# Kernel optimization log

Measured on AMD Instinct MI355X. Metric: run time of the kernel, lower is better.

The kernel has to match this reference:

```python
import jax, jax.numpy as jnp
import numpy as np

N_NODES = 100000
N_EDGES = 600000
NUM_GRAPHS = 512
IN_DIM = 128
HID = 64
HEADS = 2
NEG_SLOPE = 0.2


def gat_layer(h_in, src, dst, W, a_s, a_d, b, n_nodes):
    # W: [F_in, H*C], a_s/a_d: [H, C], b: [H*C]
    H, C = a_s.shape
    h = (h_in @ W).reshape(n_nodes, H, C)            # [N,H,C]
    alpha_src = jnp.einsum('nhc,hc->nh', h, a_s)      # [N,H]
    alpha_dst = jnp.einsum('nhc,hc->nh', h, a_d)      # [N,H]
    e = alpha_src[src] + alpha_dst[dst]               # [E,H]
    e = jnp.where(e >= 0, e, NEG_SLOPE * e)           # leaky_relu
    # segment softmax over destination node
    m = jax.ops.segment_max(e, dst, num_segments=n_nodes)
    m = jnp.where(jnp.isfinite(m), m, 0.0)
    ex = jnp.exp(e - m[dst])                          # [E,H]
    denom = jax.ops.segment_sum(ex, dst, num_segments=n_nodes)
    alpha = ex / jnp.maximum(denom[dst], 1e-16)       # [E,H]
    out = jax.ops.segment_sum(alpha[:, :, None] * h[src], dst, num_segments=n_nodes)
    return out.reshape(n_nodes, H * C) + b


def setup_inputs() -> dict:
    key = jax.random.key(0)
    ks = jax.random.split(key, 16)
    x = jax.random.normal(ks[0], (N_NODES, IN_DIM), dtype=jnp.float32)
    edge_index = jax.random.randint(ks[1], (2, N_EDGES), 0, N_NODES, dtype=jnp.int32)
    batch = jnp.sort(jax.random.randint(ks[2], (N_NODES,), 0, NUM_GRAPHS, dtype=jnp.int32))
    s = lambda *d: 1.0 / np.sqrt(d[0])
    W1 = jax.random.normal(ks[3], (IN_DIM, HEADS * HID), jnp.float32) * s(IN_DIM)
    a_src1 = jax.random.normal(ks[4], (HEADS, HID), jnp.float32) * s(HID)
    a_dst1 = jax.random.normal(ks[5], (HEADS, HID), jnp.float32) * s(HID)
    b1 = jnp.zeros((HEADS * HID,), jnp.float32)
    W2 = jax.random.normal(ks[6], (HEADS * HID, HID), jnp.float32) * s(HEADS * HID)
    a_src2 = jax.random.normal(ks[7], (1, HID), jnp.float32) * s(HID)
    a_dst2 = jax.random.normal(ks[8], (1, HID), jnp.float32) * s(HID)
    b2 = jnp.zeros((HID,), jnp.float32)
    Wf1 = jax.random.normal(ks[9], (2 * HID, HID), jnp.float32) * s(2 * HID)
    bf1 = jnp.zeros((HID,), jnp.float32)
    Wf2 = jax.random.normal(ks[10], (HID, 1), jnp.float32) * s(HID)
    bf2 = jnp.zeros((1,), jnp.float32)
    return dict(x=x, edge_index=edge_index, batch=batch, W1=W1, a_src1=a_src1,
                a_dst1=a_dst1, b1=b1, W2=W2, a_src2=a_src2, a_dst2=a_dst2, b2=b2,
                Wf1=Wf1, bf1=bf1, Wf2=Wf2, bf2=bf2)


def reference(x, edge_index, batch, W1, a_src1, a_dst1, b1, W2, a_src2, a_dst2, b2,
              Wf1, bf1, Wf2, bf2):
    n = x.shape[0]
    loops = jnp.arange(n, dtype=edge_index.dtype)
    src = jnp.concatenate([edge_index[0], loops])
    dst = jnp.concatenate([edge_index[1], loops])
    h = gat_layer(x, src, dst, W1, a_src1, a_dst1, b1, n)
    h = jax.nn.relu(h)
    h = gat_layer(h, src, dst, W2, a_src2, a_dst2, b2, n)  # [N, HID]
    # global mean + max pool per graph
    ones = jnp.ones((n,), h.dtype)
    counts = jax.ops.segment_sum(ones, batch, num_segments=NUM_GRAPHS)  # [G]
    mean = jax.ops.segment_sum(h, batch, num_segments=NUM_GRAPHS) / jnp.maximum(counts, 1.0)[:, None]
    mx = jax.ops.segment_max(h, batch, num_segments=NUM_GRAPHS)
    mx = jnp.where(counts[:, None] > 0, mx, 0.0)
    pooled = jnp.concatenate([mean, mx], axis=1)  # [G, 2*HID]
    out = jax.nn.relu(pooled @ Wf1 + bf1) @ Wf2 + bf2  # [G, 1]
    return out
```

## Files before the change

### kernel.cpp

```cpp
#include <hip/hip_runtime.h>

#define N_NODESC 100000
#define N_EDGESC 600000
#define E_TOTC   700000
#define NUM_GRAPHSC 512
#define NEG_SLOPE 0.2f
#define NEG_INF_ENC 0x007FFFFFu
#define SCAN_NB 128

typedef unsigned short ushort_t;
typedef __attribute__((ext_vector_type(8))) short bf16x8;
typedef __attribute__((ext_vector_type(4))) float f32x4;

__device__ __forceinline__ unsigned enc_f32(float f) {
    unsigned u = __float_as_uint(f);
    return (u & 0x80000000u) ? ~u : (u | 0x80000000u);
}
__device__ __forceinline__ float dec_f32(unsigned u) {
    u = (u & 0x80000000u) ? (u ^ 0x80000000u) : ~u;
    return __uint_as_float(u);
}
__device__ __forceinline__ ushort_t f32_to_bf16(float f) {
    unsigned u = __float_as_uint(f);
    return (ushort_t)((u + 0x7FFFu + ((u >> 16) & 1u)) >> 16);
}
__device__ __forceinline__ float bf16_to_f32(ushort_t h) {
    return __uint_as_float(((unsigned)h) << 16);
}
__device__ __forceinline__ unsigned pack_bf16x2(float a, float b) {
    return (unsigned)f32_to_bf16(a) | ((unsigned)f32_to_bf16(b) << 16);
}

__global__ __launch_bounds__(256) void init_all(float* __restrict__ msum,
                                                unsigned* __restrict__ mmax,
                                                float* __restrict__ cnt,
                                                int* __restrict__ deg,
                                                const float* __restrict__ W1,
                                                const float* __restrict__ W2,
                                                ushort_t* __restrict__ wPre1,
                                                ushort_t* __restrict__ wPre2) {
    int i = blockIdx.x * 256 + threadIdx.x;
    if (i < NUM_GRAPHSC * 64) { msum[i] = 0.f; mmax[i] = NEG_INF_ENC; }
    if (i < NUM_GRAPHSC) cnt[i] = 0.f;
    if (i < N_NODESC) deg[i] = 0;
    if (i < 128 * 128) {
        int n = i >> 7, k = i & 127;
        wPre1[n * 128 + k] = f32_to_bf16(W1[k * 128 + n]);
    } else if (i < 128 * 128 + 64 * 128) {
        int j = i - 128 * 128;
        int n = j >> 7, k = j & 127;
        wPre2[n * 128 + k] = f32_to_bf16(W2[k * 64 + n]);
    }
}

__global__ __launch_bounds__(256) void hist_dst(const int* __restrict__ ei,
                                                int* __restrict__ deg) {
    int e = blockIdx.x * blockDim.x + threadIdx.x;
    if (e >= E_TOTC) return;
    int d = (e < N_EDGESC) ? ei[N_EDGESC + e] : e - N_EDGESC;
    atomicAdd(&deg[d], 1);
}

__global__ __launch_bounds__(256) void scan_partial(const int* __restrict__ deg,
                                                    int* __restrict__ bsum, int n) {
    __shared__ int red[256];
    int chunk = (n + SCAN_NB - 1) / SCAN_NB;
    int lo = blockIdx.x * chunk, hi = min(lo + chunk, n);
    int s = 0;
    for (int i = lo + threadIdx.x; i < hi; i += 256) s += deg[i];
    red[threadIdx.x] = s;
    __syncthreads();
    for (int d = 128; d; d >>= 1) {
        if (threadIdx.x < d) red[threadIdx.x] += red[threadIdx.x + d];
        __syncthreads();
    }
    if (threadIdx.x == 0) bsum[blockIdx.x] = red[0];
}

__global__ __launch_bounds__(256) void scan_final(const int* __restrict__ deg,
                                                  const int* __restrict__ bsum,
                                                  int* __restrict__ off, int n) {
    __shared__ int bs[SCAN_NB];
    __shared__ int tile[256];
    __shared__ int carry;
    int t = threadIdx.x;
    if (t < SCAN_NB) bs[t] = bsum[t];
    __syncthreads();
    for (int d = 1; d < SCAN_NB; d <<= 1) {
        int v = (t >= d && t < SCAN_NB) ? bs[t - d] : 0;
        __syncthreads();
        if (t < SCAN_NB) bs[t] += v;
        __syncthreads();
    }
    if (t == 0) carry = blockIdx.x ? bs[blockIdx.x - 1] : 0;
    __syncthreads();
    int chunk = (n + SCAN_NB - 1) / SCAN_NB;
    int lo = blockIdx.x * chunk, hi = min(lo + chunk, n);
    for (int base = lo; base < hi; base += 256) {
        int i = base + t;
        int v = (i < hi) ? deg[i] : 0;
        tile[t] = v;
        __syncthreads();
        for (int d = 1; d < 256; d <<= 1) {
            int u = (t >= d) ? tile[t - d] : 0;
            __syncthreads();
            tile[t] += u;
            __syncthreads();
        }
        if (i < hi) off[i] = carry + tile[t] - v;
        __syncthreads();
        if (t == 0) carry += tile[255];
        __syncthreads();
    }
}

__global__ __launch_bounds__(256) void scatter_csr(const int* __restrict__ ei,
                                                   int* __restrict__ off,
                                                   int* __restrict__ csr) {
    int e = blockIdx.x * blockDim.x + threadIdx.x;
    if (e >= E_TOTC) return;
    int s, d;
    if (e < N_EDGESC) { s = ei[e]; d = ei[N_EDGESC + e]; } else { s = d = e - N_EDGESC; }
    int slot = atomicAdd(&off[d], 1);
    csr[slot] = s;
}

__global__ __launch_bounds__(256) void gemm1_mfma(const float* __restrict__ X,
                                                  const ushort_t* __restrict__ Wp,
                                                  ushort_t* __restrict__ Y16, int N) {
    int tid = threadIdx.x;
    int wave = tid >> 6, lane = tid & 63;
    int quad = lane >> 4, l16 = lane & 15;
    size_t node0 = (size_t)blockIdx.x * 64;

    f32x4 acc[4][2];
#pragma unroll
    for (int rt = 0; rt < 4; ++rt)
#pragma unroll
        for (int ct = 0; ct < 2; ++ct) acc[rt][ct] = (f32x4){0.f, 0.f, 0.f, 0.f};

    const ushort_t* w0p = Wp + (size_t)(16 * wave + l16) * 128;
    const ushort_t* w1p = Wp + (size_t)(64 + 16 * wave + l16) * 128;

#pragma unroll
    for (int kc = 0; kc < 4; ++kc) {
        int kb = kc * 32 + quad * 8;
        float4 xa[4], xb[4];
#pragma unroll
        for (int rt = 0; rt < 4; ++rt) {
            size_t row = node0 + rt * 16 + l16;
            if (row >= (size_t)N) row = N - 1;
            const float* xp = X + row * 128 + kb;
            xa[rt] = *(const float4*)xp;
            xb[rt] = *(const float4*)(xp + 4);
        }
        bf16x8 b0 = *(const bf16x8*)(w0p + kb);
        bf16x8 b1 = *(const bf16x8*)(w1p + kb);
#pragma unroll
        for (int rt = 0; rt < 4; ++rt) {
            union { bf16x8 v; unsigned u[4]; } af;
            af.u[0] = pack_bf16x2(xa[rt].x, xa[rt].y);
            af.u[1] = pack_bf16x2(xa[rt].z, xa[rt].w);
            af.u[2] = pack_bf16x2(xb[rt].x, xb[rt].y);
            af.u[3] = pack_bf16x2(xb[rt].z, xb[rt].w);
            acc[rt][0] = __builtin_amdgcn_mfma_f32_16x16x32_bf16(af.v, b0, acc[rt][0], 0, 0, 0);
            acc[rt][1] = __builtin_amdgcn_mfma_f32_16x16x32_bf16(af.v, b1, acc[rt][1], 0, 0, 0);
        }
    }
    unsigned* Yu = (unsigned*)Y16;
    int c = 16 * wave + l16;
#pragma unroll
    for (int rt = 0; rt < 4; ++rt)
#pragma unroll
        for (int r = 0; r < 4; ++r) {
            size_t row = node0 + rt * 16 + quad * 4 + r;
            if (row < (size_t)N)
                Yu[row * 64 + c] = pack_bf16x2(acc[rt][0][r], acc[rt][1][r]);
        }
}

__global__ __launch_bounds__(256) void gemm2_mfma(const ushort_t* __restrict__ Xb,
                                                  const ushort_t* __restrict__ Wp,
                                                  ushort_t* __restrict__ Y16, int N) {
    int tid = threadIdx.x;
    int wave = tid >> 6, lane = tid & 63;
    int quad = lane >> 4, l16 = lane & 15;
    int rbase = (wave >> 1) * 32, cbase = (wave & 1) * 32;
    size_t node0 = (size_t)blockIdx.x * 64;

    bf16x8 a[2][4];
#pragma unroll
    for (int rt = 0; rt < 2; ++rt) {
        size_t row = node0 + rbase + rt * 16 + l16;
        if (row >= (size_t)N) row = N - 1;
#pragma unroll
        for (int kc = 0; kc < 4; ++kc)
            a[rt][kc] = *(const bf16x8*)(Xb + row * 128 + kc * 32 + quad * 8);
    }

    const ushort_t* b0p = Wp + (size_t)(cbase + l16) * 128;
    const ushort_t* b1p = Wp + (size_t)(cbase + 16 + l16) * 128;

    f32x4 acc[2][2];
#pragma unroll
    for (int rt = 0; rt < 2; ++rt)
#pragma unroll
        for (int ct = 0; ct < 2; ++ct) acc[rt][ct] = (f32x4){0.f, 0.f, 0.f, 0.f};

#pragma unroll
    for (int kc = 0; kc < 4; ++kc) {
        int kb = kc * 32 + quad * 8;
        bf16x8 b0 = *(const bf16x8*)(b0p + kb);
        bf16x8 b1 = *(const bf16x8*)(b1p + kb);
#pragma unroll
        for (int rt = 0; rt < 2; ++rt) {
            acc[rt][0] = __builtin_amdgcn_mfma_f32_16x16x32_bf16(a[rt][kc], b0, acc[rt][0], 0, 0, 0);
            acc[rt][1] = __builtin_amdgcn_mfma_f32_16x16x32_bf16(a[rt][kc], b1, acc[rt][1], 0, 0, 0);
        }
    }
#pragma unroll
    for (int rt = 0; rt < 2; ++rt)
#pragma unroll
        for (int ct = 0; ct < 2; ++ct)
#pragma unroll
            for (int r = 0; r < 4; ++r) {
                size_t row = node0 + rbase + rt * 16 + quad * 4 + r;
                if (row < (size_t)N)
                    Y16[row * 64 + cbase + ct * 16 + l16] = f32_to_bf16(acc[rt][ct][r]);
            }
}

template <int H>
__global__ __launch_bounds__(256) void node_alpha(const ushort_t* __restrict__ H16,
                                                  const float* __restrict__ a_s,
                                                  const float* __restrict__ a_d,
                                                  float* __restrict__ as_out,
                                                  float* __restrict__ ad_out, int N) {
    int wid = threadIdx.x >> 6, lane = threadIdx.x & 63;
    int n = blockIdx.x * 4 + wid;
    if (n >= N) return;
    if (H == 2) {
        const unsigned* hrow = (const unsigned*)(H16 + (size_t)n * 128);
        unsigned u = hrow[lane];
        float h0 = __uint_as_float(u << 16);
        float h1 = __uint_as_float(u & 0xffff0000u);
        float ps0 = h0 * a_s[lane], pd0 = h0 * a_d[lane];
        float ps1 = h1 * a_s[64 + lane], pd1 = h1 * a_d[64 + lane];
#pragma unroll
        for (int off = 32; off; off >>= 1) {
            ps0 += __shfl_xor(ps0, off);
            pd0 += __shfl_xor(pd0, off);
            ps1 += __shfl_xor(ps1, off);
            pd1 += __shfl_xor(pd1, off);
        }
        if (lane == 0) {
            as_out[n * 2 + 0] = ps0; ad_out[n * 2 + 0] = pd0;
            as_out[n * 2 + 1] = ps1; ad_out[n * 2 + 1] = pd1;
        }
    } else {
        float hv = bf16_to_f32(H16[(size_t)n * 64 + lane]);
        float ps = hv * a_s[lane];
        float pd = hv * a_d[lane];
#pragma unroll
        for (int off = 32; off; off >>= 1) {
            ps += __shfl_xor(ps, off);
            pd += __shfl_xor(pd, off);
        }
        if (lane == 0) { as_out[n] = ps; ad_out[n] = pd; }
    }
}

template <int H, bool RELU, bool OB16>
__global__ __launch_bounds__(256) void gat_gather(const int* __restrict__ off_end,
                                                  const int* __restrict__ deg,
                                                  const int* __restrict__ csr,
                                                  const float* __restrict__ as,
                                                  const float* __restrict__ ad,
                                                  const ushort_t* __restrict__ H16,
                                                  const float* __restrict__ b,
                                                  void* __restrict__ outp, int N) {
    int lane = threadIdx.x & 63;
    int wave = threadIdx.x >> 6;
    int l = lane & 15;
    int gbase = lane & 48;
    int n = blockIdx.x * 16 + wave * 4 + (lane >> 4);
    if (n >= N) return;
    int dg = deg[n];
    int o = off_end[n] - dg;
    float adv[H];
#pragma unroll
    for (int h = 0; h < H; ++h) adv[h] = ad[n * H + h];

    float acc[H][4], den[H];
#pragma unroll
    for (int h = 0; h < H; ++h) {
        den[h] = 0.f;
#pragma unroll
        for (int q = 0; q < 4; ++q) acc[h][q] = 0.f;
    }

    const unsigned* Hu = (const unsigned*)H16;

    for (int base = 0; base < dg; base += 16) {
        int i = base + l;
        bool valid = i < dg;
        int s = valid ? csr[o + i] : 0;
        float v[H];
        if (H == 2) {
            float2 p = valid ? ((const float2*)as)[s] : make_float2(0.f, 0.f);
            v[0] = p.x + adv[0];
            v[H - 1] = p.y + adv[H - 1];
        } else {
            v[0] = valid ? as[s] + adv[0] : 0.f;
        }
#pragma unroll
        for (int h = 0; h < H; ++h) {
            float e = v[h] >= 0.f ? v[h] : NEG_SLOPE * v[h];
            v[h] = valid ? __expf(e) : 0.f;
            den[h] += v[h];
        }
        int wpk = (H == 2) ? (int)pack_bf16x2(v[0], v[H - 1])
                           : (int)__float_as_uint(v[0]);
        int cnt = min(dg - base, 16);
        int cnt4 = (cnt + 3) & ~3;
        for (int j = 0; j < cnt4; j += 4) {
#pragma unroll
            for (int u = 0; u < 4; ++u) {
                int src = gbase + j + u;
                int sj = __shfl(s, src);
                int wp = __shfl(wpk, src);
                if (H == 2) {
                    float w0 = __uint_as_float(((unsigned)wp) << 16);
                    float w1 = __uint_as_float(((unsigned)wp) & 0xffff0000u);
                    uint4 hu = *(const uint4*)(Hu + (size_t)sj * 64 + l * 4);
                    acc[0][0] += w0 * __uint_as_float(hu.x << 16);
                    acc[H - 1][0] += w1 * __uint_as_float(hu.x & 0xffff0000u);
                    acc[0][1] += w0 * __uint_as_float(hu.y << 16);
                    acc[H - 1][1] += w1 * __uint_as_float(hu.y & 0xffff0000u);
                    acc[0][2] += w0 * __uint_as_float(hu.z << 16);
                    acc[H - 1][2] += w1 * __uint_as_float(hu.z & 0xffff0000u);
                    acc[0][3] += w0 * __uint_as_float(hu.w << 16);
                    acc[H - 1][3] += w1 * __uint_as_float(hu.w & 0xffff0000u);
                } else {
                    float w0 = __uint_as_float((unsigned)wp);
                    uint2 hu = *(const uint2*)((const unsigned*)(H16 + (size_t)sj * 64) + l * 2);
                    acc[0][0] += w0 * __uint_as_float(hu.x << 16);
                    acc[0][1] += w0 * __uint_as_float(hu.x & 0xffff0000u);
                    acc[0][2] += w0 * __uint_as_float(hu.y << 16);
                    acc[0][3] += w0 * __uint_as_float(hu.y & 0xffff0000u);
                }
            }
        }
    }
#pragma unroll
    for (int h = 0; h < H; ++h) {
#pragma unroll
        for (int sh = 8; sh; sh >>= 1) den[h] += __shfl_xor(den[h], sh);
    }
    if (H == 2) {
        float4 b0 = *(const float4*)(b + l * 4);
        float4 b1 = *(const float4*)(b + 64 + l * 4);
        float r0[4], r1[4];
        float id0 = 1.f / fmaxf(den[0], 1e-16f);
        float id1 = 1.f / fmaxf(den[H - 1], 1e-16f);
        r0[0] = acc[0][0] * id0 + b0.x; r0[1] = acc[0][1] * id0 + b0.y;
        r0[2] = acc[0][2] * id0 + b0.z; r0[3] = acc[0][3] * id0 + b0.w;
        r1[0] = acc[H - 1][0] * id1 + b1.x; r1[1] = acc[H - 1][1] * id1 + b1.y;
        r1[2] = acc[H - 1][2] * id1 + b1.z; r1[3] = acc[H - 1][3] * id1 + b1.w;
        if (RELU) {
#pragma unroll
            for (int q = 0; q < 4; ++q) { r0[q] = fmaxf(r0[q], 0.f); r1[q] = fmaxf(r1[q], 0.f); }
        }
        ushort_t* outb = (ushort_t*)outp;
        uint2 p0 = make_uint2(pack_bf16x2(r0[0], r0[1]), pack_bf16x2(r0[2], r0[3]));
        uint2 p1 = make_uint2(pack_bf16x2(r1[0], r1[1]), pack_bf16x2(r1[2], r1[3]));
        *(uint2*)(outb + (size_t)n * 128 + l * 4) = p0;
        *(uint2*)(outb + (size_t)n * 128 + 64 + l * 4) = p1;
    } else {
        float4 bv = *(const float4*)(b + l * 4);
        float id0 = 1.f / fmaxf(den[0], 1e-16f);
        float4 r;
        r.x = acc[0][0] * id0 + bv.x; r.y = acc[0][1] * id0 + bv.y;
        r.z = acc[0][2] * id0 + bv.z; r.w = acc[0][3] * id0 + bv.w;
        if (RELU) { r.x = fmaxf(r.x, 0.f); r.y = fmaxf(r.y, 0.f);
                    r.z = fmaxf(r.z, 0.f); r.w = fmaxf(r.w, 0.f); }
        *(float4*)((float*)outp + (size_t)n * 64 + l * 4) = r;
    }
}

__global__ __launch_bounds__(256) void pool_nodes(const float* __restrict__ h2,
                                                  const int* __restrict__ batch,
                                                  float* __restrict__ msum,
                                                  unsigned* __restrict__ mmax,
                                                  float* __restrict__ cnt, int N) {
    int wid = threadIdx.x >> 6, lane = threadIdx.x & 63;
    int n0 = (blockIdx.x * 4 + wid) * 64;
    if (n0 >= N) return;
    int n1 = min(n0 + 64, N);
    int curg = batch[n0];
    float s = 0.f, m = -1e30f;
    int c = 0;
    for (int n = n0; n < n1; ++n) {
        int g = batch[n];
        float v = h2[(size_t)n * 64 + lane];
        if (g != curg) {
            atomicAdd(&msum[curg * 64 + lane], s);
            atomicMax(&mmax[curg * 64 + lane], enc_f32(m));
            if (lane == 0) atomicAdd(&cnt[curg], (float)c);
            s = 0.f; m = -1e30f; c = 0; curg = g;
        }
        s += v;
        m = fmaxf(m, v);
        ++c;
    }
    atomicAdd(&msum[curg * 64 + lane], s);
    atomicMax(&mmax[curg * 64 + lane], enc_f32(m));
    if (lane == 0) atomicAdd(&cnt[curg], (float)c);
}

__global__ __launch_bounds__(64) void mlp_head(const float* __restrict__ msum,
                                               const unsigned* __restrict__ mmax,
                                               const float* __restrict__ cnt,
                                               const float* __restrict__ Wf1,
                                               const float* __restrict__ bf1,
                                               const float* __restrict__ Wf2,
                                               const float* __restrict__ bf2,
                                               float* __restrict__ out) {
    __shared__ float pooled[128];
    int g = blockIdx.x, lane = threadIdx.x;
    float c = cnt[g];
    pooled[lane] = msum[g * 64 + lane] / fmaxf(c, 1.0f);
    pooled[64 + lane] = (c > 0.f) ? dec_f32(mmax[g * 64 + lane]) : 0.f;
    __syncthreads();
    float acc = bf1[lane];
#pragma unroll
    for (int k = 0; k < 128; ++k) acc += pooled[k] * Wf1[k * 64 + lane];
    acc = fmaxf(acc, 0.f);
    float r = acc * Wf2[lane];
#pragma unroll
    for (int off = 32; off; off >>= 1) r += __shfl_xor(r, off);
    if (lane == 0) out[g] = r + bf2[0];
}

extern "C" void kernel_launch(void* const* d_in, const int* in_sizes, int n_in,
                              void* d_out, int out_size, void* d_ws, size_t ws_size,
                              hipStream_t stream) {
    const float* x    = (const float*)d_in[0];
    const int*   ei   = (const int*)d_in[1];
    const int*   batch= (const int*)d_in[2];
    const float* W1   = (const float*)d_in[3];
    const float* as1  = (const float*)d_in[4];
    const float* ad1  = (const float*)d_in[5];
    const float* b1   = (const float*)d_in[6];
    const float* W2   = (const float*)d_in[7];
    const float* as2  = (const float*)d_in[8];
    const float* ad2  = (const float*)d_in[9];
    const float* b2   = (const float*)d_in[10];
    const float* Wf1  = (const float*)d_in[11];
    const float* bf1  = (const float*)d_in[12];
    const float* Wf2  = (const float*)d_in[13];
    const float* bf2  = (const float*)d_in[14];
    float* out = (float*)d_out;

    const size_t N = N_NODESC;
    float* ws = (float*)d_ws;
    ushort_t* h16_1 = (ushort_t*)ws;
    ushort_t* out1b = (ushort_t*)(ws + N * 64);
    ushort_t* h16_2 = (ushort_t*)(ws + N * 128);
    float*    out2  = ws + N * 160;
    float*    small = ws + N * 224;
    float*    as1b = small;
    float*    ad1b = small + 2 * N;
    float*    as2b = small + 4 * N;
    float*    ad2b = small + 5 * N;
    float*    msum = small + 6 * N;
    unsigned* mmax = (unsigned*)(small + 6 * N + 512 * 64);
    float*    cntb = small + 6 * N + 2 * 512 * 64;
    int* ip  = (int*)(small + 6 * N + 2 * 512 * 64 + 512);
    int* deg  = ip;
    int* off  = ip + N;
    int* csr  = ip + 2 * N;
    int* bsum = ip + 2 * N + E_TOTC;
    ushort_t* wPre1 = (ushort_t*)(bsum + SCAN_NB);
    ushort_t* wPre2 = wPre1 + 128 * 128;

    init_all<<<(N_NODESC + 255) / 256, 256, 0, stream>>>(msum, mmax, cntb, deg,
                                                         W1, W2, wPre1, wPre2);

    hist_dst<<<(E_TOTC + 255) / 256, 256, 0, stream>>>(ei, deg);
    scan_partial<<<SCAN_NB, 256, 0, stream>>>(deg, bsum, N);
    scan_final<<<SCAN_NB, 256, 0, stream>>>(deg, bsum, off, N);
    scatter_csr<<<(E_TOTC + 255) / 256, 256, 0, stream>>>(ei, off, csr);

    const int NBLK64 = (N_NODESC + 63) / 64;
    const int NBLK16 = (N_NODESC + 15) / 16;

    gemm1_mfma<<<NBLK64, 256, 0, stream>>>(x, wPre1, h16_1, N);
    node_alpha<2><<<(N + 3) / 4, 256, 0, stream>>>(h16_1, as1, ad1, as1b, ad1b, N);
    gat_gather<2, true, true><<<NBLK16, 256, 0, stream>>>(off, deg, csr, as1b,
                                                          ad1b, h16_1, b1, out1b, N);

    gemm2_mfma<<<NBLK64, 256, 0, stream>>>(out1b, wPre2, h16_2, N);
    node_alpha<1><<<(N + 3) / 4, 256, 0, stream>>>(h16_2, as2, ad2, as2b, ad2b, N);
    gat_gather<1, false, false><<<NBLK16, 256, 0, stream>>>(off, deg, csr, as2b,
                                                            ad2b, h16_2, b2, out2, N);

    pool_nodes<<<(N + 255) / 256, 256, 0, stream>>>(out2, batch, msum, mmax, cntb, N);
    mlp_head<<<NUM_GRAPHSC, 64, 0, stream>>>(msum, mmax, cntb, Wf1, bf1, Wf2, bf2, out);
}
```

Before: 347.4 us.

## Repartition gemm1 so each wave owns 16 rows and all output columns

The first-layer GEMM is remapped so each wave computes 16 node rows across all 128 output columns, instead of 64 rows across a 32-column slice. Each X row is now read and converted to bf16 by only one wave, where before all four waves read and converted the same X tile. The trade-off is that every wave reloads the whole weight matrix from global/L2 memory, and the per-thread accumulator count stays the same. The output packing pairs column tiles ct and ct+4 to keep the interleaved bf16x2 layout the later stages expect.

```diff
diff --git a/kernel.cpp b/kernel.cpp
--- a/kernel.cpp
+++ b/kernel.cpp
@@ -131,52 +131,47 @@
     int tid = threadIdx.x;
     int wave = tid >> 6, lane = tid & 63;
     int quad = lane >> 4, l16 = lane & 15;
-    size_t node0 = (size_t)blockIdx.x * 64;
-
-    f32x4 acc[4][2];
-#pragma unroll
-    for (int rt = 0; rt < 4; ++rt)
-#pragma unroll
-        for (int ct = 0; ct < 2; ++ct) acc[rt][ct] = (f32x4){0.f, 0.f, 0.f, 0.f};
-
-    const ushort_t* w0p = Wp + (size_t)(16 * wave + l16) * 128;
-    const ushort_t* w1p = Wp + (size_t)(64 + 16 * wave + l16) * 128;
+    size_t node0 = (size_t)blockIdx.x * 64 + wave * 16;
+
+    size_t arow = node0 + l16;
+    if (arow >= (size_t)N) arow = N - 1;
+    const float* xp = X + arow * 128;
+    float4 xa[4], xb[4];
+#pragma unroll
+    for (int kc = 0; kc < 4; ++kc) {
+        xa[kc] = *(const float4*)(xp + kc * 32 + quad * 8);
+        xb[kc] = *(const float4*)(xp + kc * 32 + quad * 8 + 4);
+    }
+
+    f32x4 acc[8];
+#pragma unroll
+    for (int ct = 0; ct < 8; ++ct) acc[ct] = (f32x4){0.f, 0.f, 0.f, 0.f};
 
 #pragma unroll
     for (int kc = 0; kc < 4; ++kc) {
         int kb = kc * 32 + quad * 8;
-        float4 xa[4], xb[4];
-#pragma unroll
-        for (int rt = 0; rt < 4; ++rt) {
-            size_t row = node0 + rt * 16 + l16;
-            if (row >= (size_t)N) row = N - 1;
-            const float* xp = X + row * 128 + kb;
-            xa[rt] = *(const float4*)xp;
-            xb[rt] = *(const float4*)(xp + 4);
-        }
-        bf16x8 b0 = *(const bf16x8*)(w0p + kb);
-        bf16x8 b1 = *(const bf16x8*)(w1p + kb);
-#pragma unroll
-        for (int rt = 0; rt < 4; ++rt) {
-            union { bf16x8 v; unsigned u[4]; } af;
-            af.u[0] = pack_bf16x2(xa[rt].x, xa[rt].y);
-            af.u[1] = pack_bf16x2(xa[rt].z, xa[rt].w);
-            af.u[2] = pack_bf16x2(xb[rt].x, xb[rt].y);
-            af.u[3] = pack_bf16x2(xb[rt].z, xb[rt].w);
-            acc[rt][0] = __builtin_amdgcn_mfma_f32_16x16x32_bf16(af.v, b0, acc[rt][0], 0, 0, 0);
-            acc[rt][1] = __builtin_amdgcn_mfma_f32_16x16x32_bf16(af.v, b1, acc[rt][1], 0, 0, 0);
+        union { bf16x8 v; unsigned u[4]; } af;
+        af.u[0] = pack_bf16x2(xa[kc].x, xa[kc].y);
+        af.u[1] = pack_bf16x2(xa[kc].z, xa[kc].w);
+        af.u[2] = pack_bf16x2(xb[kc].x, xb[kc].y);
+        af.u[3] = pack_bf16x2(xb[kc].z, xb[kc].w);
+#pragma unroll
+        for (int ct = 0; ct < 8; ++ct) {
+            bf16x8 b = *(const bf16x8*)(Wp + (size_t)(ct * 16 + l16) * 128 + kb);
+            acc[ct] = __builtin_amdgcn_mfma_f32_16x16x32_bf16(af.v, b, acc[ct], 0, 0, 0);
         }
     }
     unsigned* Yu = (unsigned*)Y16;
-    int c = 16 * wave + l16;
-#pragma unroll
-    for (int rt = 0; rt < 4; ++rt)
+#pragma unroll
+    for (int ct = 0; ct < 4; ++ct) {
+        int c = ct * 16 + l16;
 #pragma unroll
         for (int r = 0; r < 4; ++r) {
-            size_t row = node0 + rt * 16 + quad * 4 + r;
+            size_t row = node0 + quad * 4 + r;
             if (row < (size_t)N)
-                Yu[row * 64 + c] = pack_bf16x2(acc[rt][0][r], acc[rt][1][r]);
-        }
+                Yu[row * 64 + c] = pack_bf16x2(acc[ct][r], acc[ct + 4][r]);
+        }
+    }
 }
 
 __global__ __launch_bounds__(256) void gemm2_mfma(const ushort_t* __restrict__ Xb,
```

Measured after the change: 342.4 us. Within noise of the previous version (-1.4%).
